# Optimization experiments

Hardware: AMD Instinct MI355X
Metric: run time of the kernel (lower is better)

The kernel has to match this reference:

```python
import jax, jax.numpy as jnp
import numpy as np
from jax import lax

SUBBANDS = 4
TAPS = 64
BETA = 9.0


def _qmf_filter():
    # scipy.signal.kaiser(M, beta) == np.kaiser(M, beta)
    h = np.kaiser(TAPS + 1, BETA)
    h = h / np.sum(h)
    n = np.arange(TAPS + 1)
    filt = [h * np.cos((2 * k + 1) * np.pi * n / (2 * SUBBANDS) + (-1) ** k * np.pi / 4)
            for k in range(SUBBANDS)]
    return np.asarray(filt, dtype=np.float32)  # [S, TAPS+1]


def setup_inputs() -> dict:
    key = jax.random.key(0)
    x = jax.random.normal(key, (16, 1, 524288), dtype=jnp.float32)
    qmf = jnp.asarray(_qmf_filter())
    return {"x": x, "qmf": qmf}


def reference(x, qmf):
    S = SUBBANDS
    pad = TAPS // 2  # 32
    # --- analysis: full conv then ::S decimation == strided conv (identical outputs) ---
    wa = qmf[:, None, :]  # [S, 1, TAPS+1] (OIW)
    sub = lax.conv_general_dilated(
        x, wa, window_strides=(S,), padding=[(pad, pad)],
        dimension_numbers=("NCH", "OIH", "NCH"))  # [B, S, T//S]
    # --- synthesis: zero-stuff upsample by S then conv, summed over subbands.
    # lhs_dilation=S inserts the zeros; right pad extra S-1 to match the
    # explicit x_up buffer (3 trailing zeros after the last sample).
    # Summing the S per-subband convs == one conv with S input channels.
    ws = qmf[None, :, :]  # [1, S, TAPS+1]
    y = lax.conv_general_dilated(
        sub, ws, window_strides=(1,), padding=[(pad, pad + S - 1)],
        lhs_dilation=(S,), dimension_numbers=("NCH", "OIH", "NCH"))  # [B, 1, T]
    return y
```

## Files before the change

### kernel.cpp

```cpp
#include <hip/hip_runtime.h>

#define LEN 524288
#define LSUB 131072
#define BATCH 16

constexpr double cabs_d(double a) { return a < 0 ? -a : a; }
constexpr double csqrt_d(double a) {
    double x = (a > 1.0) ? a : 1.0;
    for (int i = 0; i < 48; i++) x = 0.5 * (x + a / x);
    return x;
}
constexpr double i0_d(double x) {
    double t = 1.0, s = 1.0;
    for (int m = 1; m < 50; m++) { double u = x / (2.0 * m); t *= u * u; s += t; }
    return s;
}
struct Tbl {
    float f[4][65];
    float C[4][129];
};
constexpr Tbl make_tbl() {
    Tbl T{};
    double h[65] = {};
    double sum = 0.0;
    const double ib = i0_d(9.0);
    for (int n = 0; n < 65; n++) {
        double r = (n - 32.0) / 32.0;
        double a = 1.0 - r * r; if (a < 0) a = 0;
        h[n] = i0_d(9.0 * csqrt_d(a)) / ib;
        sum += h[n];
    }
    for (int n = 0; n < 65; n++) h[n] /= sum;
    const double S2 = csqrt_d(2.0);
    const double c1 = 0.5 * csqrt_d(2.0 + S2);
    const double c2 = 0.5 * S2;
    const double c3 = 0.5 * csqrt_d(2.0 - S2);
    const double ct[16] = {1,c1,c2,c3,0,-c3,-c2,-c1,-1,-c1,-c2,-c3,0,c3,c2,c1};
    double f[4][65] = {};
    for (int k = 0; k < 4; k++)
        for (int n = 0; n < 65; n++) {
            int m = ((2 * k + 1) * n + ((k & 1) ? 14 : 2)) & 15;
            f[k][n] = h[n] * ct[m];
            T.f[k][n] = (float)f[k][n];
        }
    double Cd[4][129] = {};
    for (int p = 0; p < 4; p++)
        for (int dd = -64; dd <= 64; dd++) {
            double a = 0.0;
            for (int k = 0; k < 4; k++)
                for (int j = -8; j <= 8; j++) {
                    int ia = 4 * j + 32 - p, ib2 = dd - 4 * j + 32;
                    if (ia >= 0 && ia <= 64 && ib2 >= 0 && ib2 <= 64)
                        a += f[k][ia] * f[k][ib2];
                }
            Cd[p][dd + 64] = a;
        }
    for (int p = 0; p < 4; p++) {
        double budget = 2e-8;
        while (true) {
            int best = -1; double bv = 1e30;
            for (int d = 0; d < 129; d++) {
                double c = cabs_d(Cd[p][d]);
                if (c > 0.0 && c < bv) { bv = c; best = d; }
            }
            if (best < 0 || bv * bv > budget) break;
            budget -= bv * bv;
            Cd[p][best] = 0.0;
        }
        for (int d = 0; d < 129; d++) T.C[p][d] = (float)Cd[p][d];
    }
    return T;
}
static constexpr Tbl TBL = make_tbl();

__device__ __forceinline__ float getc(const float4& v, int c) {
    switch (c) { case 0: return v.x; case 1: return v.y; case 2: return v.z; default: return v.w; }
}
__device__ __forceinline__ float cpv(int p, int dlt) {
    return (dlt < -64 || dlt > 64) ? 0.0f : TBL.C[p][dlt + 64];
}

template <bool SAFE>
__device__ __forceinline__ void compute_granule(const float4* __restrict__ xb4, int g,
                                                float (&acc)[4]) {
    #pragma unroll
    for (int e = -16; e <= 16; e++) {
        float4 v;
        if (SAFE) {
            int gg = g + e;
            v = (gg >= 0 && gg < LSUB) ? xb4[gg] : make_float4(0.f, 0.f, 0.f, 0.f);
        } else {
            v = xb4[g + e];
        }
        #pragma unroll
        for (int c = 0; c < 4; c++) {
            const int par = c & 1;
            const float w0 = cpv(par,     4 * e + c);
            const float w1 = cpv(par + 2, 4 * e + c);
            const float xv = getc(v, c);
            if (w0 != 0.f) acc[par]     = fmaf(w0, xv, acc[par]);
            if (w1 != 0.f) acc[par + 2] = fmaf(w1, xv, acc[par + 2]);
        }
    }
}

__device__ void left_fix_g(const float* __restrict__ xb, int g, float (&acc)[4]) {
    #pragma unroll
    for (int mi = 0; mi < 8; mi++) {
        const int m = mi - 8;
        float s0 = 0.f, s1 = 0.f, s2 = 0.f, s3 = 0.f;
        #pragma unroll
        for (int n = 64 - 4 * mi; n <= 64; n++) {
            float xv = xb[4 * m - 32 + n];
            s0 = fmaf(TBL.f[0][n], xv, s0);
            s1 = fmaf(TBL.f[1][n], xv, s1);
            s2 = fmaf(TBL.f[2][n], xv, s2);
            s3 = fmaf(TBL.f[3][n], xv, s3);
        }
        #pragma unroll
        for (int p = 0; p < 4; p++) {
            int np = 4 * (m - g) + 32 - p;
            if (np >= 0 && np <= 64) {
                float w = TBL.f[0][np] * s0 + TBL.f[1][np] * s1 +
                          TBL.f[2][np] * s2 + TBL.f[3][np] * s3;
                acc[p] -= w;
            }
        }
    }
}

__device__ void right_fix_g(const float* __restrict__ xb, int g, float (&acc)[4]) {
    #pragma unroll
    for (int mi = 0; mi < 8; mi++) {
        const int m = LSUB + mi;
        float s0 = 0.f, s1 = 0.f, s2 = 0.f, s3 = 0.f;
        #pragma unroll
        for (int n = 0; n <= 31 - 4 * mi; n++) {
            float xv = xb[4 * m - 32 + n];
            s0 = fmaf(TBL.f[0][n], xv, s0);
            s1 = fmaf(TBL.f[1][n], xv, s1);
            s2 = fmaf(TBL.f[2][n], xv, s2);
            s3 = fmaf(TBL.f[3][n], xv, s3);
        }
        #pragma unroll
        for (int p = 0; p < 4; p++) {
            int np = 4 * (m - g) + 32 - p;
            if (np >= 0 && np <= 64) {
                float w = TBL.f[0][np] * s0 + TBL.f[1][np] * s1 +
                          TBL.f[2][np] * s2 + TBL.f[3][np] * s3;
                acc[p] -= w;
            }
        }
    }
}

__global__ __launch_bounds__(256, 4) void pqmf_direct(const float* __restrict__ x,
                                                      float* __restrict__ y) {
    const int idx = blockIdx.x * 256 + threadIdx.x;
    const int g = idx & (LSUB - 1);
    const int b = idx >> 17;
    const float* xb = x + (size_t)b * LEN;
    const float4* xb4 = reinterpret_cast<const float4*>(xb);

    float acc[4] = {0.f, 0.f, 0.f, 0.f};
    if (g >= 16 && g < LSUB - 16) {
        compute_granule<false>(xb4, g, acc);
    } else {
        compute_granule<true>(xb4, g, acc);
        if (g <= 8) left_fix_g(xb, g, acc);
        if (g >= LSUB - 9) right_fix_g(xb, g, acc);
    }
    reinterpret_cast<float4*>(y + (size_t)b * LEN)[g] =
        make_float4(acc[0], acc[1], acc[2], acc[3]);
}

extern "C" void kernel_launch(void* const* d_in, const int* in_sizes, int n_in,
                              void* d_out, int out_size, void* d_ws, size_t ws_size,
                              hipStream_t stream) {
    const float* x = (const float*)d_in[0];
    float* y = (float*)d_out;
    dim3 blk(256);
    dim3 grd(BATCH * LSUB / 256);
    pqmf_direct<<<grd, blk, 0, stream>>>(x, y);
}
```

Baseline: 90.89 us.

## Compute four adjacent output granules per thread with register reuse and LDS-staged stores

Each thread now produces four consecutive float4 output granules, loading 36 input float4s instead of 4×33. This lets the loaded values be reused across outputs in registers and cuts redundant global and L1 loads. Results are staged through a swizzled per-wave LDS buffer so the global stores stay coalesced. The cost is more registers per thread (16 accumulators plus unrolled loads), which may hurt occupancy, and a quarter as many threads in the grid.

Result: slower. 260.2 us (+186.3%).

```diff
diff --git a/kernel.cpp b/kernel.cpp
--- a/kernel.cpp
+++ b/kernel.cpp
@@ -79,30 +79,7 @@
 __device__ __forceinline__ float cpv(int p, int dlt) {
     return (dlt < -64 || dlt > 64) ? 0.0f : TBL.C[p][dlt + 64];
 }
-
-template <bool SAFE>
-__device__ __forceinline__ void compute_granule(const float4* __restrict__ xb4, int g,
-                                                float (&acc)[4]) {
-    #pragma unroll
-    for (int e = -16; e <= 16; e++) {
-        float4 v;
-        if (SAFE) {
-            int gg = g + e;
-            v = (gg >= 0 && gg < LSUB) ? xb4[gg] : make_float4(0.f, 0.f, 0.f, 0.f);
-        } else {
-            v = xb4[g + e];
-        }
-        #pragma unroll
-        for (int c = 0; c < 4; c++) {
-            const int par = c & 1;
-            const float w0 = cpv(par,     4 * e + c);
-            const float w1 = cpv(par + 2, 4 * e + c);
-            const float xv = getc(v, c);
-            if (w0 != 0.f) acc[par]     = fmaf(w0, xv, acc[par]);
-            if (w1 != 0.f) acc[par + 2] = fmaf(w1, xv, acc[par + 2]);
-        }
-    }
-}
+__device__ __forceinline__ int swz(int g) { return g ^ ((g >> 3) & 7); }
 
 __device__ void left_fix_g(const float* __restrict__ xb, int g, float (&acc)[4]) {
     #pragma unroll
@@ -121,9 +98,8 @@
         for (int p = 0; p < 4; p++) {
             int np = 4 * (m - g) + 32 - p;
             if (np >= 0 && np <= 64) {
-                float w = TBL.f[0][np] * s0 + TBL.f[1][np] * s1 +
+                acc[p] -= TBL.f[0][np] * s0 + TBL.f[1][np] * s1 +
                           TBL.f[2][np] * s2 + TBL.f[3][np] * s3;
-                acc[p] -= w;
             }
         }
     }
@@ -146,32 +122,78 @@
         for (int p = 0; p < 4; p++) {
             int np = 4 * (m - g) + 32 - p;
             if (np >= 0 && np <= 64) {
-                float w = TBL.f[0][np] * s0 + TBL.f[1][np] * s1 +
+                acc[p] -= TBL.f[0][np] * s0 + TBL.f[1][np] * s1 +
                           TBL.f[2][np] * s2 + TBL.f[3][np] * s3;
-                acc[p] -= w;
-            }
-        }
-    }
-}
-
-__global__ __launch_bounds__(256, 4) void pqmf_direct(const float* __restrict__ x,
-                                                      float* __restrict__ y) {
-    const int idx = blockIdx.x * 256 + threadIdx.x;
-    const int g = idx & (LSUB - 1);
-    const int b = idx >> 17;
+            }
+        }
+    }
+}
+
+template <bool SAFE>
+__device__ __forceinline__ void compute4(const float4* __restrict__ xb4, int g0,
+                                         float (&acc)[4][4]) {
+    #pragma unroll
+    for (int j = 0; j < 36; j++) {
+        const int gg = g0 - 16 + j;
+        float4 v;
+        if (SAFE) {
+            v = (gg >= 0 && gg < LSUB) ? xb4[gg] : make_float4(0.f, 0.f, 0.f, 0.f);
+        } else {
+            v = xb4[gg];
+        }
+        #pragma unroll
+        for (int o = 0; o < 4; o++) {
+            const int e = j - 16 - o;
+            if (e < -16 || e > 16) continue;
+            #pragma unroll
+            for (int c = 0; c < 4; c++) {
+                const int par = c & 1;
+                const float w0 = cpv(par,     4 * e + c);
+                const float w1 = cpv(par + 2, 4 * e + c);
+                const float xv = getc(v, c);
+                if (w0 != 0.f) acc[o][par]     = fmaf(w0, xv, acc[o][par]);
+                if (w1 != 0.f) acc[o][par + 2] = fmaf(w1, xv, acc[o][par + 2]);
+            }
+        }
+    }
+}
+
+__global__ __launch_bounds__(256, 4) void pqmf_direct4(const float* __restrict__ x,
+                                                       float* __restrict__ y) {
+    __shared__ float4 sbuf[4][256];
+
+    const int t = threadIdx.x;
+    const int wv = t >> 6, l = t & 63;
+    const int b = blockIdx.x >> 7;
+    const int B = blockIdx.x & 127;
+    const int grp = B * 256 + t;
+    const int g0 = 4 * grp;
     const float* xb = x + (size_t)b * LEN;
     const float4* xb4 = reinterpret_cast<const float4*>(xb);
 
-    float acc[4] = {0.f, 0.f, 0.f, 0.f};
-    if (g >= 16 && g < LSUB - 16) {
-        compute_granule<false>(xb4, g, acc);
+    float acc[4][4] = {};
+    if (g0 >= 16 && g0 + 19 < LSUB) {
+        compute4<false>(xb4, g0, acc);
     } else {
-        compute_granule<true>(xb4, g, acc);
-        if (g <= 8) left_fix_g(xb, g, acc);
-        if (g >= LSUB - 9) right_fix_g(xb, g, acc);
-    }
-    reinterpret_cast<float4*>(y + (size_t)b * LEN)[g] =
-        make_float4(acc[0], acc[1], acc[2], acc[3]);
+        compute4<true>(xb4, g0, acc);
+        #pragma unroll
+        for (int o = 0; o < 4; o++) {
+            if (g0 + o <= 8)           left_fix_g(xb, g0 + o, acc[o]);
+            if (g0 + o >= LSUB - 9)    right_fix_g(xb, g0 + o, acc[o]);
+        }
+    }
+
+    #pragma unroll
+    for (int o = 0; o < 4; o++)
+        sbuf[wv][swz(4 * l + o)] = make_float4(acc[o][0], acc[o][1], acc[o][2], acc[o][3]);
+    asm volatile("s_waitcnt lgkmcnt(0)" ::: "memory");
+    __builtin_amdgcn_wave_barrier();
+
+    float4* yb4 = reinterpret_cast<float4*>(y + (size_t)b * LEN);
+    const int wbase = 4 * (B * 256 + (t & ~63));
+    #pragma unroll
+    for (int o = 0; o < 4; o++)
+        yb4[wbase + 64 * o + l] = sbuf[wv][swz(64 * o + l)];
 }
 
 extern "C" void kernel_launch(void* const* d_in, const int* in_sizes, int n_in,
@@ -180,6 +202,6 @@
     const float* x = (const float*)d_in[0];
     float* y = (float*)d_out;
     dim3 blk(256);
-    dim3 grd(BATCH * LSUB / 256);
-    pqmf_direct<<<grd, blk, 0, stream>>>(x, y);
-}
+    dim3 grd(BATCH * (LSUB / 4) / 256);
+    pqmf_direct4<<<grd, blk, 0, stream>>>(x, y);
+}
```
